# Optimization experiments

Hardware: AMD Instinct MI355X
Metric: run time of the kernel (lower is better)

## Reference

```python
import jax, jax.numpy as jnp
import numpy as np

N_NODES = 5
B, C, H, W = 4, 256, 32, 32
THRESH = 0.3
EPS = 1e-12


def setup_inputs() -> dict:
    key = jax.random.key(0)
    k1, k2, k3, k4 = jax.random.split(key, 4)
    x = jax.random.normal(k1, (N_NODES, B, C, H, W), dtype=jnp.float32)
    w = jax.random.normal(k2, (N_NODES, N_NODES), dtype=jnp.float32)
    # 5 stacked conv1x1 'experts': Conv2d(2C -> C, k=1) weight [C,2C] + bias [C]
    conv_w = jax.random.normal(k3, (N_NODES, C, 2 * C), dtype=jnp.float32) * 0.02
    conv_b = jax.random.normal(k4, (N_NODES, C), dtype=jnp.float32) * 0.02
    return {"x": x, "w": w, "conv_w": conv_w, "conv_b": conv_b}


def reference(x, w, conv_w, conv_b):
    # x: [N, B, C, H, W] -- the list of N node feature maps stacked
    N, b, c, h, ww = x.shape
    P = b * c * h * ww  # 'pixels' = total element count of one node tensor

    # conv_i(cat(node_j, node_i + node_j)) splits into W1@node_j + W2@(node_i+node_j) + b_i
    W1 = conv_w[:, :, :c]          # [N, C, C] acts on node_j
    W2 = conv_w[:, :, c:]          # [N, C, C] acts on node_i + node_j
    A = W1 + W2                    # combined weight on node_j

    term_j = jnp.einsum('ick,jbkhw->ijbchw', A, x)    # [N,N,B,C,H,W]
    term_i = jnp.einsum('ick,ibkhw->ibchw', W2, x)    # [N,B,C,H,W]
    target = term_j + term_i[:, None] + conv_b[:, None, None, :, None, None]
    distance = x[None, :] - target                    # distance[i,j] = node_j - conv_i(...)

    # edge_list[:, i, j] = flatten(distance[i, j])  -> [P, N, N]
    edge = distance.reshape(N, N, P).transpose(2, 0, 1)

    # new_edge = edge * w; sigmoid; threshold at 0.3; L2-normalize over dim=2 (j axis)
    e = jax.nn.sigmoid(edge * w)
    e = jnp.where(e > THRESH, e, jnp.zeros_like(e))
    norm = jnp.sqrt(jnp.sum(e * e, axis=2, keepdims=True))
    e = e / jnp.maximum(norm, EPS)

    # node matrix: [P, N] of flattened node features; fuse h[p,i] = sum_j e[p,i,j]*node[p,j]
    node = x.reshape(N, P).T
    hmat = jnp.einsum('pij,pj->pi', e, node)          # [P, N]
    return hmat.T.reshape(N, b, c, h, ww)
```

## Files before the change

### kernel.cpp

```cpp
#include <hip/hip_runtime.h>
#include <cmath>

#define NN  5
#define BB  4
#define CCH 256
#define HWD 1024
#define THRESH_V 0.3f
#define EPS_V 1e-12f


#define CT 64
#define WT 64
#define KC 8
#define APAD 68
#define SPAD 68

#define W2T_OFF (NN * CCH * CCH)

#define XS_FLOATS (NN * KC * WT)
#define AS_OFF    XS_FLOATS
#define W2S_OFF   (AS_OFF + KC * APAD)
#define SMEM_FLOATS (W2S_OFF + KC * APAD)

__global__ void fub_prep(const float* __restrict__ conv_w, float* __restrict__ ws)
{
    const int t = blockIdx.x * 256 + threadIdx.x;
    if (t >= NN * CCH * 64) return;
    const int c4 = (t & 63) << 2;
    const int k  = (t >> 6) & 255;
    const int i  = t >> 14;
    float s1[4], s2[4];
#pragma unroll
    for (int cc = 0; cc < 4; ++cc) {
        const float* p = conv_w + (size_t)(i * CCH + c4 + cc) * (2 * CCH) + k;
        const float w1 = p[0];
        const float w2 = p[CCH];
        s1[cc] = w1 + w2;
        s2[cc] = w2;
    }
    float* At  = ws + (size_t)(i * CCH + k) * CCH + c4;
    float* W2t = ws + W2T_OFF + (size_t)(i * CCH + k) * CCH + c4;
    *(float4*)At  = make_float4(s1[0], s1[1], s1[2], s1[3]);
    *(float4*)W2t = make_float4(s2[0], s2[1], s2[2], s2[3]);
}

__global__ __launch_bounds__(384, 3)
void fub_main(const float* __restrict__ x, const float* __restrict__ wmat,
              const float* __restrict__ ws, const float* __restrict__ conv_b,
              float* __restrict__ out)
{
    __shared__ __align__(16) float smem[SMEM_FLOATS];
    float* Xs  = smem;
    float* As  = smem + AS_OFF;
    float* W2s = smem + W2S_OFF;
    float* Es  = smem;

    const int tid  = threadIdx.x;
    const int wv   = tid >> 6;
    const int lane = tid & 63;

    const int wg  = blockIdx.x;
    int L = (wg & 7) * 160 + (wg >> 3);
    const int i   = L % 5;  L /= 5;
    const int ct  = L & 3;  L >>= 2;
    const int b   = L & 3;  L >>= 2;
    const int hwt = L;

    const int c0  = ct * CT;
    const int hw0 = hwt * WT;

    const int lr = (lane >> 3) << 3;
    const int lc = (lane & 7)  << 3;

    const int jx = (wv < NN) ? wv : i;
    const float* Ms = (wv == 5) ? W2s : As;
    const float* Mb = Ms + lr;
    const float* Xb = Xs + jx * (KC * WT) + lc;

    float acc[8][8];
#pragma unroll
    for (int r = 0; r < 8; ++r)
#pragma unroll
        for (int c = 0; c < 8; ++c) acc[r][c] = 0.0f;

    for (int k0 = 0; k0 < CCH; k0 += KC) {
#pragma unroll
        for (int it = 0; it < 3; ++it) {
            const int t = tid + it * 384;
            if (t < 640) {
                const int j   = t >> 7;
                const int rem = t & 127;
                const int kk  = rem >> 4;
                const int q4  = (rem & 15) << 2;
                const float4 v = *(const float4*)(
                    x + (size_t)((j * BB + b) * CCH + k0 + kk) * HWD + hw0 + q4);
                *(float4*)(Xs + j * (KC * WT) + kk * WT + q4) = v;
            } else if (t < 896) {
                const int u   = t - 640;
                const int tbl = u >> 7;
                const int rem = u & 127;
                const int kk  = rem >> 4;
                const int c4  = (rem & 15) << 2;
                const float4 v = *(const float4*)(
                    ws + (size_t)(tbl ? W2T_OFF : 0)
                       + (size_t)(i * CCH + k0 + kk) * CCH + c0 + c4);
                *(float4*)((tbl ? W2s : As) + kk * APAD + c4) = v;
            }
        }
        __syncthreads();

#pragma unroll
        for (int kk = 0; kk < KC; ++kk) {
            const float4 a0 = *(const float4*)(Mb + kk * APAD);
            const float4 a1 = *(const float4*)(Mb + kk * APAD + 4);
            const float4 x0 = *(const float4*)(Xb + kk * WT);
            const float4 x1 = *(const float4*)(Xb + kk * WT + 4);
            const float ar[8] = {a0.x, a0.y, a0.z, a0.w, a1.x, a1.y, a1.z, a1.w};
            const float xc[8] = {x0.x, x0.y, x0.z, x0.w, x1.x, x1.y, x1.z, x1.w};
#pragma unroll
            for (int r = 0; r < 8; ++r)
#pragma unroll
                for (int c = 0; c < 8; ++c)
                    acc[r][c] = fmaf(ar[r], xc[c], acc[r][c]);
        }
        __syncthreads();
    }

    float wrow[NN];
#pragma unroll
    for (int j = 0; j < NN; ++j) wrow[j] = wmat[i * NN + j];

    const int g = lane >> 3;

#pragma unroll
    for (int rh = 0; rh < 8; ++rh) {
        if (g == rh) {
            float* Eb = Es + wv * (KC * SPAD) + lc;
#pragma unroll
            for (int r = 0; r < 8; ++r) {
                *(float4*)(Eb + r * SPAD) =
                    make_float4(acc[r][0], acc[r][1], acc[r][2], acc[r][3]);
                *(float4*)(Eb + r * SPAD + 4) =
                    make_float4(acc[r][4], acc[r][5], acc[r][6], acc[r][7]);
            }
        }
        __syncthreads();

        if (tid < 256) {
            const int row  = tid >> 5;
            const int col2 = (tid & 31) << 1;
            const int c    = c0 + rh * 8 + row;
            const float bias = conv_b[i * CCH + c];

            const float2 T = *(const float2*)(Es + 5 * (KC * SPAD) + row * SPAD + col2);
            const float Tv[2] = {T.x, T.y};

            float num[2] = {0.f, 0.f};
            float sq [2] = {0.f, 0.f};
#pragma unroll
            for (int j = 0; j < NN; ++j) {
                const float2 s  = *(const float2*)(Es + j * (KC * SPAD) + row * SPAD + col2);
                const float2 xj = *(const float2*)(
                    x + (size_t)((j * BB + b) * CCH + c) * HWD + hw0 + col2);
                const float sv[2] = {s.x, s.y};
                const float xv[2] = {xj.x, xj.y};
#pragma unroll
                for (int cc = 0; cc < 2; ++cc) {
                    const float target = sv[cc] + Tv[cc] + bias;
                    const float dist   = xv[cc] - target;
                    const float z      = dist * wrow[j];
                    float e = 1.0f / (1.0f + expf(-z));
                    e = (e > THRESH_V) ? e : 0.0f;
                    sq[cc]  = fmaf(e, e, sq[cc]);
                    num[cc] = fmaf(e, xv[cc], num[cc]);
                }
            }
            float2 res;
            res.x = num[0] / fmaxf(sqrtf(sq[0]), EPS_V);
            res.y = num[1] / fmaxf(sqrtf(sq[1]), EPS_V);
            *(float2*)(out + (size_t)((i * BB + b) * CCH + c) * HWD + hw0 + col2) = res;
        }
        __syncthreads();
    }
}

extern "C" void kernel_launch(void* const* d_in, const int* in_sizes, int n_in,
                              void* d_out, int out_size, void* d_ws, size_t ws_size,
                              hipStream_t stream) {
    const float* x      = (const float*)d_in[0];
    const float* w      = (const float*)d_in[1];
    const float* conv_w = (const float*)d_in[2];
    const float* conv_b = (const float*)d_in[3];
    float* out = (float*)d_out;
    float* ws  = (float*)d_ws;

    fub_prep<<<dim3(320), dim3(256), 0, stream>>>(conv_w, ws);

    fub_main<<<dim3(1280), dim3(384), 0, stream>>>(x, w, ws, conv_b, out);
}
```

Baseline: 354.5 us.

## Drop LDS staging in GEMM, load operands directly with register prefetch and smaller tiles

Removes the shared-memory staging of x and weight tiles and the per-chunk barriers, so each lane reads its A and X vectors straight from global memory (relying on cache) with a one-step register prefetch. The hw tile is halved to 32, giving each thread an 8x4 accumulator and doubling the grid to 2560 blocks. The epilogue is rearranged to 16-row passes. The aim is to cut barrier and LDS traffic and raise occupancy, at the cost of redundant global/L2 loads across lanes and waves and less reuse per loaded operand.

```diff
diff --git a/kernel.cpp b/kernel.cpp
--- a/kernel.cpp
+++ b/kernel.cpp
@@ -10,17 +10,11 @@
 
 
 #define CT 64
-#define WT 64
-#define KC 8
-#define APAD 68
-#define SPAD 68
+#define WT 32
+#define SPAD 36
 
 #define W2T_OFF (NN * CCH * CCH)
-
-#define XS_FLOATS (NN * KC * WT)
-#define AS_OFF    XS_FLOATS
-#define W2S_OFF   (AS_OFF + KC * APAD)
-#define SMEM_FLOATS (W2S_OFF + KC * APAD)
+#define SMEM_FLOATS (6 * 16 * SPAD)
 
 __global__ void fub_prep(const float* __restrict__ conv_w, float* __restrict__ ws)
 {
@@ -49,18 +43,14 @@
               const float* __restrict__ ws, const float* __restrict__ conv_b,
               float* __restrict__ out)
 {
-    __shared__ __align__(16) float smem[SMEM_FLOATS];
-    float* Xs  = smem;
-    float* As  = smem + AS_OFF;
-    float* W2s = smem + W2S_OFF;
-    float* Es  = smem;
+    __shared__ __align__(16) float Es[SMEM_FLOATS];
 
     const int tid  = threadIdx.x;
     const int wv   = tid >> 6;
     const int lane = tid & 63;
 
     const int wg  = blockIdx.x;
-    int L = (wg & 7) * 160 + (wg >> 3);
+    int L = (wg & 7) * 320 + (wg >> 3);
     const int i   = L % 5;  L /= 5;
     const int ct  = L & 3;  L >>= 2;
     const int b   = L & 3;  L >>= 2;
@@ -70,109 +60,97 @@
     const int hw0 = hwt * WT;
 
     const int lr = (lane >> 3) << 3;
-    const int lc = (lane & 7)  << 3;
+    const int lc = (lane & 7)  << 2;
 
     const int jx = (wv < NN) ? wv : i;
-    const float* Ms = (wv == 5) ? W2s : As;
-    const float* Mb = Ms + lr;
-    const float* Xb = Xs + jx * (KC * WT) + lc;
+    const float* Ap = ws + (size_t)((wv == NN) ? W2T_OFF : 0)
+                         + (size_t)i * CCH * CCH + c0 + lr;
+    const float* Xp = x + (size_t)((jx * BB + b) * CCH) * HWD + hw0 + lc;
 
-    float acc[8][8];
+    float acc[8][4];
 #pragma unroll
     for (int r = 0; r < 8; ++r)
 #pragma unroll
-        for (int c = 0; c < 8; ++c) acc[r][c] = 0.0f;
+        for (int c = 0; c < 4; ++c) acc[r][c] = 0.0f;
 
-    for (int k0 = 0; k0 < CCH; k0 += KC) {
+    float4 a0 = *(const float4*)Ap;
+    float4 a1 = *(const float4*)(Ap + 4);
+    float4 xv = *(const float4*)Xp;
+
+#pragma unroll 4
+    for (int k = 0; k < 255; ++k) {
+        const float* An = Ap + CCH;
+        const float* Xn = Xp + HWD;
+        const float4 na0 = *(const float4*)An;
+        const float4 na1 = *(const float4*)(An + 4);
+        const float4 nx  = *(const float4*)Xn;
+
+        const float ar[8] = {a0.x, a0.y, a0.z, a0.w, a1.x, a1.y, a1.z, a1.w};
+        const float xc[4] = {xv.x, xv.y, xv.z, xv.w};
 #pragma unroll
-        for (int it = 0; it < 3; ++it) {
-            const int t = tid + it * 384;
-            if (t < 640) {
-                const int j   = t >> 7;
-                const int rem = t & 127;
-                const int kk  = rem >> 4;
-                const int q4  = (rem & 15) << 2;
-                const float4 v = *(const float4*)(
-                    x + (size_t)((j * BB + b) * CCH + k0 + kk) * HWD + hw0 + q4);
-                *(float4*)(Xs + j * (KC * WT) + kk * WT + q4) = v;
-            } else if (t < 896) {
-                const int u   = t - 640;
-                const int tbl = u >> 7;
-                const int rem = u & 127;
-                const int kk  = rem >> 4;
-                const int c4  = (rem & 15) << 2;
-                const float4 v = *(const float4*)(
-                    ws + (size_t)(tbl ? W2T_OFF : 0)
-                       + (size_t)(i * CCH + k0 + kk) * CCH + c0 + c4);
-                *(float4*)((tbl ? W2s : As) + kk * APAD + c4) = v;
-            }
-        }
-        __syncthreads();
+        for (int r = 0; r < 8; ++r)
+#pragma unroll
+            for (int c = 0; c < 4; ++c)
+                acc[r][c] = fmaf(ar[r], xc[c], acc[r][c]);
 
+        a0 = na0; a1 = na1; xv = nx;
+        Ap = An; Xp = Xn;
+    }
+    {
+        const float ar[8] = {a0.x, a0.y, a0.z, a0.w, a1.x, a1.y, a1.z, a1.w};
+        const float xc[4] = {xv.x, xv.y, xv.z, xv.w};
 #pragma unroll
-        for (int kk = 0; kk < KC; ++kk) {
-            const float4 a0 = *(const float4*)(Mb + kk * APAD);
-            const float4 a1 = *(const float4*)(Mb + kk * APAD + 4);
-            const float4 x0 = *(const float4*)(Xb + kk * WT);
-            const float4 x1 = *(const float4*)(Xb + kk * WT + 4);
-            const float ar[8] = {a0.x, a0.y, a0.z, a0.w, a1.x, a1.y, a1.z, a1.w};
-            const float xc[8] = {x0.x, x0.y, x0.z, x0.w, x1.x, x1.y, x1.z, x1.w};
+        for (int r = 0; r < 8; ++r)
 #pragma unroll
-            for (int r = 0; r < 8; ++r)
-#pragma unroll
-                for (int c = 0; c < 8; ++c)
-                    acc[r][c] = fmaf(ar[r], xc[c], acc[r][c]);
-        }
-        __syncthreads();
+            for (int c = 0; c < 4; ++c)
+                acc[r][c] = fmaf(ar[r], xc[c], acc[r][c]);
     }
+
+    const int rhme  = lr >> 4;
+    const int rbase = lr & 15;
 
     float wrow[NN];
 #pragma unroll
     for (int j = 0; j < NN; ++j) wrow[j] = wmat[i * NN + j];
 
-    const int g = lane >> 3;
-
 #pragma unroll
-    for (int rh = 0; rh < 8; ++rh) {
-        if (g == rh) {
-            float* Eb = Es + wv * (KC * SPAD) + lc;
+    for (int rh = 0; rh < 4; ++rh) {
+        if (rhme == rh) {
+            float* Eb = Es + wv * (16 * SPAD) + lc;
 #pragma unroll
-            for (int r = 0; r < 8; ++r) {
-                *(float4*)(Eb + r * SPAD) =
+            for (int r = 0; r < 8; ++r)
+                *(float4*)(Eb + (rbase + r) * SPAD) =
                     make_float4(acc[r][0], acc[r][1], acc[r][2], acc[r][3]);
-                *(float4*)(Eb + r * SPAD + 4) =
-                    make_float4(acc[r][4], acc[r][5], acc[r][6], acc[r][7]);
-            }
         }
         __syncthreads();
 
         if (tid < 256) {
-            const int row  = tid >> 5;
-            const int col2 = (tid & 31) << 1;
-            const int c    = c0 + rh * 8 + row;
+            const int row  = tid >> 4;
+            const int col2 = (tid & 15) << 1;
+            const int c    = c0 + rh * 16 + row;
             const float bias = conv_b[i * CCH + c];
 
-            const float2 T = *(const float2*)(Es + 5 * (KC * SPAD) + row * SPAD + col2);
+            const float2 T = *(const float2*)(Es + 5 * (16 * SPAD) + row * SPAD + col2);
             const float Tv[2] = {T.x, T.y};
 
             float num[2] = {0.f, 0.f};
             float sq [2] = {0.f, 0.f};
 #pragma unroll
             for (int j = 0; j < NN; ++j) {
-                const float2 s  = *(const float2*)(Es + j * (KC * SPAD) + row * SPAD + col2);
+                const float2 s  = *(const float2*)(Es + j * (16 * SPAD) + row * SPAD + col2);
                 const float2 xj = *(const float2*)(
                     x + (size_t)((j * BB + b) * CCH + c) * HWD + hw0 + col2);
                 const float sv[2] = {s.x, s.y};
-                const float xv[2] = {xj.x, xj.y};
+                const float xvv[2] = {xj.x, xj.y};
 #pragma unroll
                 for (int cc = 0; cc < 2; ++cc) {
                     const float target = sv[cc] + Tv[cc] + bias;
-                    const float dist   = xv[cc] - target;
+                    const float dist   = xvv[cc] - target;
                     const float z      = dist * wrow[j];
                     float e = 1.0f / (1.0f + expf(-z));
                     e = (e > THRESH_V) ? e : 0.0f;
                     sq[cc]  = fmaf(e, e, sq[cc]);
-                    num[cc] = fmaf(e, xv[cc], num[cc]);
+                    num[cc] = fmaf(e, xvv[cc], num[cc]);
                 }
             }
             float2 res;
@@ -196,5 +174,5 @@
 
     fub_prep<<<dim3(320), dim3(256), 0, stream>>>(conv_w, ws);
 
-    fub_main<<<dim3(1280), dim3(384), 0, stream>>>(x, w, ws, conv_b, out);
+    fub_main<<<dim3(2560), dim3(384), 0, stream>>>(x, w, ws, conv_b, out);
 }
```

Result: slower. 464.8 us (+31.1%).
